# Optimization experiments

Measured on AMD Instinct MI355X. Metric: run time of the kernel, lower is better.

The kernel has to match this reference:

```python
import jax, jax.numpy as jnp
import numpy as np
from jax.scipy.linalg import solve_triangular


def setup_inputs() -> dict:
    B, L, H, Dv, Mh = 32, 1024, 12, 64, 64
    hdim = H * Dv
    key = jax.random.key(0)
    ks = jax.random.split(key, 6)
    x = jax.random.normal(ks[0], (B, L, hdim), jnp.float32)
    W_qv = jax.random.normal(ks[1], (2 * H * Dv, hdim), jnp.float32) * 0.02
    log_sf = jnp.zeros((H, 1), jnp.float32)
    log_ls = jnp.zeros((H, Dv), jnp.float32)
    log_sigma2 = jnp.asarray(-2.0, jnp.float32)
    omega = jax.random.normal(ks[2], (H, Dv, Mh), jnp.float32)
    omega_half, _ = jnp.linalg.qr(omega)  # per-head orthonormal columns, Dv >= Mh
    phase = 2.0 * np.pi * jax.random.uniform(ks[3], (H, Mh), jnp.float32)
    W_O_w = jax.random.normal(ks[4], (hdim, hdim), jnp.float32) * 0.02
    W_O_b = jnp.zeros((hdim,), jnp.float32)
    eps = jax.random.normal(ks[5], (B, H, 1, L, Dv), jnp.float32)  # sample_size=1
    return dict(x=x, W_qv=W_qv, log_sf=log_sf, log_ls=log_ls,
                log_sigma2=log_sigma2, omega_half=omega_half, phase=phase,
                W_O_w=W_O_w, W_O_b=W_O_b, eps=eps)


def reference(x, W_qv, log_sf, log_ls, log_sigma2, omega_half, phase, W_O_w, W_O_b, eps):
    B, L, hdim = x.shape
    H, Dv, Mh = omega_half.shape
    M = 2 * Mh
    jitter = 1e-06
    # fc_qv (no bias), split into q / v per head: [B,H,L,Dv]
    qv = (x @ W_qv.T).reshape(B, L, H, 2 * Dv).transpose(0, 2, 1, 3)
    q, v = qv[..., :Dv], qv[..., Dv:]
    # RFF feature map (ard kernel): phi [B,H,L,M]
    scale = jnp.sqrt(2.0) * jnp.exp(-log_ls)                  # [H,Dv]
    omega = omega_half * scale[:, :, None]                    # [H,Dv,Mh]
    proj = jnp.einsum('bhld,hdm->bhlm', q, omega) + phase[None, :, None, :]
    phi = jnp.concatenate([jnp.cos(proj), jnp.sin(proj)], axis=-1)
    amp = jnp.sqrt(jnp.exp(log_sf))[None, :, None, :]         # [1,H,1,1]
    phi = amp * phi * (1.0 / np.sqrt(M))
    sigma2 = jnp.exp(log_sigma2)
    # Gram + regularized Cholesky (upper R with A = R^T R; lower Lc = R^T)
    G = jnp.einsum('bhlm,bhln->bhmn', phi, phi)               # [B,H,M,M]
    I = jnp.eye(M, dtype=x.dtype)
    A = G + (sigma2 + jitter) * I
    Lc = jnp.linalg.cholesky(A)                               # lower
    R = jnp.swapaxes(Lc, -1, -2)                              # upper
    # whitened features: tQ = (R^-T phi^T)^T  (phi_q == phi_k)
    tQ = jnp.swapaxes(solve_triangular(Lc, jnp.swapaxes(phi, -1, -2), lower=True), -1, -2)
    S = jnp.einsum('bhlm,bhld->bhmd', tQ, v)                  # [B,H,M,Dv]
    mean_feat = jnp.einsum('bhlm,bhmd->bhld', tQ, S)          # [B,H,L,Dv]
    var_scalar = sigma2 * jnp.sum(tQ ** 2, axis=-1, keepdims=True)  # [B,H,L,1]
    std = jnp.sqrt(jnp.clip(var_scalar, 0.0))
    # sampling: [B,H,Smp,L,Dv] -> [B,Smp,L,H*Dv]
    samples = mean_feat[:, :, None] + std[:, :, None] * eps
    Smp = eps.shape[2]
    samples = samples.transpose(0, 2, 3, 1, 4).reshape(B, Smp, L, H * Dv)
    samples = samples @ W_O_w.T + W_O_b  # W_O (dropout = identity)
    # exact feature-space KL
    W_star = solve_triangular(R, S, lower=False)              # [B,H,M,Dv]
    mu_norm2 = jnp.sum(W_star ** 2, axis=(-2, -1))
    R_inv = solve_triangular(R, jnp.broadcast_to(I, A.shape), lower=False)
    tr_Ainv = jnp.sum(R_inv ** 2, axis=(-2, -1))
    logdetA = 2.0 * jnp.sum(jnp.log(jnp.diagonal(R, axis1=-2, axis2=-1)), axis=-1)
    k = M * Dv
    KL_bh = 0.5 * (Dv * sigma2 * tr_Ainv + mu_norm2 - k
                   - Dv * (M * jnp.log(sigma2) - logdetA))
    kl = KL_bh.sum(axis=1).mean()
    return samples, kl
```

## Files before the change

kernel.cpp:

```cpp
#include <hip/hip_runtime.h>
#include <hip/hip_bf16.h>
#include <math.h>

#define B_   32
#define L_   1024
#define H_   12
#define DV   64
#define MH   64
#define MM   128
#define HD   768
#define BH_  384

typedef unsigned int  uint32;
typedef unsigned short ushort16;
typedef __attribute__((ext_vector_type(4))) float f32x4;
typedef __attribute__((ext_vector_type(8))) short bf16x8;

__device__ __forceinline__ float bf2f(uint32 u) {
  return __uint_as_float(u << 16);
}
__device__ __forceinline__ ushort16 f2bf(float f) {
  uint32 x = __float_as_uint(f);
  x += 0x7FFFu + ((x >> 16) & 1u);
  return (ushort16)(x >> 16);
}
__device__ __forceinline__ uint32 pack2bf(float a, float b) {
  return (uint32)f2bf(a) | ((uint32)f2bf(b) << 16);
}

__global__ __launch_bounds__(256)
void k0_prep(const float* __restrict__ x, const float* __restrict__ Wqv,
             const float* __restrict__ omega_half, const float* __restrict__ log_ls,
             ushort16* __restrict__ xbf, ushort16* __restrict__ wqvbf,
             ushort16* __restrict__ omTbf, float* __restrict__ klbuf) {
  size_t i0 = (size_t)blockIdx.x * 256 + threadIdx.x;
  size_t stride = (size_t)gridDim.x * 256;
  for (size_t i = i0; i < (size_t)25165824 / 4; i += stride) {
    float4 v = ((const float4*)x)[i];
    uint2 w; w.x = pack2bf(v.x, v.y); w.y = pack2bf(v.z, v.w);
    ((uint2*)xbf)[i] = w;
  }
  for (size_t i = i0; i < (size_t)1179648 / 4; i += stride) {
    float4 v = ((const float4*)Wqv)[i];
    uint2 w; w.x = pack2bf(v.x, v.y); w.y = pack2bf(v.z, v.w);
    ((uint2*)wqvbf)[i] = w;
  }
  if (blockIdx.x < H_) {
    int h = blockIdx.x;
    for (int e = threadIdx.x; e < MH * DV; e += blockDim.x) {
      int m = e >> 6, d = e & 63;
      float scale = 1.41421356237f * expf(-log_ls[h * DV + d]);
      omTbf[h * MH * DV + m * DV + d] = f2bf(omega_half[h * DV * MH + d * MH + m] * scale);
    }
  }
  if (blockIdx.x == 0) {
    for (int e = threadIdx.x; e < BH_; e += blockDim.x) klbuf[e] = 0.f;
  }
}

__global__ __launch_bounds__(256)
void k1_qv_mfma(const ushort16* __restrict__ xbf, const ushort16* __restrict__ wqvbf,
                ushort16* __restrict__ qv) {
  __shared__ ushort16 As[128 * 40];
  __shared__ ushort16 Bs[128 * 40];
  int tid = threadIdx.x;
  int h  = blockIdx.x % 12;
  int tm = blockIdx.x / 12;
  int m0 = tm * 128;
  int n0 = h * 128;
  int wave = tid >> 6, lane = tid & 63;
  int wy = wave >> 1, wx = wave & 1;
  int mlane = lane & 15, q = lane >> 4;
  f32x4 acc[4][4];
#pragma unroll
  for (int i = 0; i < 4; i++)
#pragma unroll
    for (int j = 0; j < 4; j++) acc[i][j] = (f32x4){0.f, 0.f, 0.f, 0.f};

  int c0 = tid, c1 = tid + 256;
  int rowA0 = c0 >> 2, ka0 = (c0 & 3) * 8;
  int rowA1 = c1 >> 2, ka1 = (c1 & 3) * 8;

  for (int k0 = 0; k0 < HD; k0 += 32) {
    __syncthreads();
    uint4 a0 = *(const uint4*)&xbf[(size_t)(m0 + rowA0) * HD + k0 + ka0];
    uint4 a1 = *(const uint4*)&xbf[(size_t)(m0 + rowA1) * HD + k0 + ka1];
    uint4 b0 = *(const uint4*)&wqvbf[(size_t)(n0 + rowA0) * HD + k0 + ka0];
    uint4 b1 = *(const uint4*)&wqvbf[(size_t)(n0 + rowA1) * HD + k0 + ka1];
    *(uint4*)&As[rowA0 * 40 + ka0] = a0;
    *(uint4*)&As[rowA1 * 40 + ka1] = a1;
    *(uint4*)&Bs[rowA0 * 40 + ka0] = b0;
    *(uint4*)&Bs[rowA1 * 40 + ka1] = b1;
    __syncthreads();
    bf16x8 av[4], bv[4];
#pragma unroll
    for (int i = 0; i < 4; i++)
      av[i] = *(const bf16x8*)&As[(wy * 64 + i * 16 + mlane) * 40 + q * 8];
#pragma unroll
    for (int j = 0; j < 4; j++)
      bv[j] = *(const bf16x8*)&Bs[(wx * 64 + j * 16 + mlane) * 40 + q * 8];
#pragma unroll
    for (int i = 0; i < 4; i++)
#pragma unroll
      for (int j = 0; j < 4; j++)
        acc[i][j] = __builtin_amdgcn_mfma_f32_16x16x32_bf16(av[i], bv[j], acc[i][j], 0, 0, 0);
  }
#pragma unroll
  for (int i = 0; i < 4; i++) {
#pragma unroll
    for (int e = 0; e < 4; e++) {
      int gm = m0 + wy * 64 + i * 16 + q * 4 + e;
      int b = gm >> 10, l = gm & 1023;
      ushort16* dst = qv + ((((size_t)(b * 12 + h) << 10) | (unsigned)l) << 7);
#pragma unroll
      for (int j = 0; j < 4; j++) {
        int c = wx * 64 + j * 16 + mlane;
        dst[c] = f2bf(acc[i][j][e]);
      }
    }
  }
}

__global__ __launch_bounds__(256)
void k2_gram_mfma(const ushort16* __restrict__ qv, const ushort16* __restrict__ omTbf,
                  const float* __restrict__ phase, const float* __restrict__ log_sf,
                  char* __restrict__ Gbase, float* __restrict__ Cws) {
  __shared__ ushort16 PhT[128 * 136];
  __shared__ ushort16 vT[64 * 136];
  __shared__ float phaseS[MH];
  int bh = blockIdx.x;
  int h = bh % H_;
  int tid = threadIdx.x;
  int wave = tid >> 6, lane = tid & 63;
  int ml = lane & 15, qq = lane >> 4;
  if (tid < MH) phaseS[tid] = phase[h * MH + tid];
  float amp = sqrtf(expf(log_sf[h])) * 0.08838834764831845f;
  const ushort16* qp = qv + (size_t)bh * L_ * MM;
  const ushort16* Om = omTbf + h * MH * DV;
  f32x4 gacc[2][8];
  f32x4 cacc[2][4];
#pragma unroll
  for (int i = 0; i < 2; i++) {
#pragma unroll
    for (int j = 0; j < 8; j++) gacc[i][j] = (f32x4){0.f, 0.f, 0.f, 0.f};
#pragma unroll
    for (int j = 0; j < 4; j++) cacc[i][j] = (f32x4){0.f, 0.f, 0.f, 0.f};
  }
  __syncthreads();

  for (int l0 = 0; l0 < L_; l0 += 128) {
    f32x4 pacc[2][4];
#pragma unroll
    for (int i = 0; i < 2; i++)
#pragma unroll
      for (int j = 0; j < 4; j++) pacc[i][j] = (f32x4){0.f, 0.f, 0.f, 0.f};
#pragma unroll
    for (int k = 0; k < 2; k++) {
      bf16x8 af[2], bfm[4];
#pragma unroll
      for (int i = 0; i < 2; i++)
        af[i] = *(const bf16x8*)&qp[(size_t)(l0 + wave * 32 + i * 16 + ml) * MM + k * 32 + qq * 8];
#pragma unroll
      for (int j = 0; j < 4; j++)
        bfm[j] = *(const bf16x8*)&Om[(j * 16 + ml) * DV + k * 32 + qq * 8];
#pragma unroll
      for (int i = 0; i < 2; i++)
#pragma unroll
        for (int j = 0; j < 4; j++)
          pacc[i][j] = __builtin_amdgcn_mfma_f32_16x16x32_bf16(af[i], bfm[j], pacc[i][j], 0, 0, 0);
    }
    for (int u = tid; u < 1024; u += 256) {
      int row = u >> 3, g = u & 7;
      uint4 w = *(const uint4*)&qp[(size_t)(l0 + row) * MM + 64 + g * 8];
      vT[(g * 8 + 0) * 136 + row] = (ushort16)(w.x & 0xffffu);
      vT[(g * 8 + 1) * 136 + row] = (ushort16)(w.x >> 16);
      vT[(g * 8 + 2) * 136 + row] = (ushort16)(w.y & 0xffffu);
      vT[(g * 8 + 3) * 136 + row] = (ushort16)(w.y >> 16);
      vT[(g * 8 + 4) * 136 + row] = (ushort16)(w.z & 0xffffu);
      vT[(g * 8 + 5) * 136 + row] = (ushort16)(w.z >> 16);
      vT[(g * 8 + 6) * 136 + row] = (ushort16)(w.w & 0xffffu);
      vT[(g * 8 + 7) * 136 + row] = (ushort16)(w.w >> 16);
    }
#pragma unroll
    for (int i = 0; i < 2; i++)
#pragma unroll
      for (int j = 0; j < 4; j++)
#pragma unroll
        for (int e = 0; e < 4; e++) {
          int l = wave * 32 + i * 16 + qq * 4 + e;
          int m = j * 16 + ml;
          float s = pacc[i][j][e] + phaseS[m];
          float sv, cv;
          sincosf(s, &sv, &cv);
          PhT[m * 136 + l]        = f2bf(amp * cv);
          PhT[(MH + m) * 136 + l] = f2bf(amp * sv);
        }
    __syncthreads();
#pragma unroll
    for (int k = 0; k < 4; k++) {
      bf16x8 af[2];
#pragma unroll
      for (int i = 0; i < 2; i++)
        af[i] = *(const bf16x8*)&PhT[(wave * 32 + i * 16 + ml) * 136 + k * 32 + qq * 8];
#pragma unroll
      for (int j = 0; j < 8; j++) {
        bf16x8 bfr = *(const bf16x8*)&PhT[(j * 16 + ml) * 136 + k * 32 + qq * 8];
#pragma unroll
        for (int i = 0; i < 2; i++)
          gacc[i][j] = __builtin_amdgcn_mfma_f32_16x16x32_bf16(af[i], bfr, gacc[i][j], 0, 0, 0);
      }
#pragma unroll
      for (int j = 0; j < 4; j++) {
        bf16x8 bvr = *(const bf16x8*)&vT[(j * 16 + ml) * 136 + k * 32 + qq * 8];
#pragma unroll
        for (int i = 0; i < 2; i++)
          cacc[i][j] = __builtin_amdgcn_mfma_f32_16x16x32_bf16(af[i], bvr, cacc[i][j], 0, 0, 0);
      }
    }
    __syncthreads();
  }
  float* Gp = (float*)(Gbase + (size_t)bh * 65536);
#pragma unroll
  for (int i = 0; i < 2; i++)
#pragma unroll
    for (int e = 0; e < 4; e++) {
      int m = wave * 32 + i * 16 + qq * 4 + e;
#pragma unroll
      for (int j = 0; j < 8; j++) Gp[m * MM + j * 16 + ml] = gacc[i][j][e];
    }
  float* Cp = Cws + (size_t)bh * MM * DV;
#pragma unroll
  for (int i = 0; i < 2; i++)
#pragma unroll
    for (int e = 0; e < 4; e++) {
      int m = wave * 32 + i * 16 + qq * 4 + e;
#pragma unroll
      for (int j = 0; j < 4; j++) Cp[m * DV + j * 16 + ml] = cacc[i][j][e];
    }
}

#define LB_(i,k) LBs[((i) << 7) + (((k) + (i)) & 127)]

__global__ __launch_bounds__(256)
void k3_factor(char* __restrict__ Gbase,
               const float* __restrict__ log_sigma2, float* __restrict__ klbuf) {
  __shared__ float LBs[MM * MM];
  int bh = blockIdx.x;
  int tid = threadIdx.x;
  float ls = log_sigma2[0];
  float sigma2 = expf(ls);
  float cjit = sigma2 + 1e-6f;
  const float* Gp = (const float*)(Gbase + (size_t)bh * 65536);
  for (int e = tid; e < MM * MM; e += 256) {
    int m = e >> 7, n = e & 127;
    float g = Gp[e];
    if (m == n) g += cjit;
    LB_(m, n) = g;
  }
  float klp = 0.f;

  for (int P = 0; P < 8; P++) {
    int p0 = P * 16;
    __syncthreads();
    if (tid < 16) {
      int t = tid;
      float r[16];
#pragma unroll
      for (int k = 0; k < 16; k++) r[k] = LB_(p0 + t, p0 + k);
#pragma unroll
      for (int j = 0; j < 16; j++) {
        float djj = __shfl(r[j], j);
        float sd = sqrtf(djj);
        float rinv = 1.f / sd;
        if (t == j) r[j] = sd;
        else if (t > j) r[j] *= rinv;
#pragma unroll
        for (int k2 = 0; k2 < 16; k2++) {
          if (k2 > j) {
            float lkj = __shfl(r[j], k2);
            if (t >= k2) r[k2] = fmaf(-r[j], lkj, r[k2]);
          }
        }
      }
#pragma unroll
      for (int k = 0; k < 16; k++) if (k <= t) LB_(p0 + t, p0 + k) = r[k];
      klp += 64.f * logf(r[t]);
    }
    __syncthreads();
    int NR = 112 - p0;
    if (NR > 0 && tid < NR) {
      int gi = p0 + 16 + tid;
      float a[16];
#pragma unroll
      for (int k = 0; k < 16; k++) a[k] = LB_(gi, p0 + k);
#pragma unroll
      for (int j = 0; j < 16; j++) {
        float inv = 1.f / LB_(p0 + j, p0 + j);
        a[j] *= inv;
#pragma unroll
        for (int k = 0; k < 16; k++)
          if (k > j) a[k] = fmaf(-a[j], LB_(p0 + k, p0 + j), a[k]);
      }
#pragma unroll
      for (int k = 0; k < 16; k++) LB_(gi, p0 + k) = a[k];
    }
    __syncthreads();
    int S = NR;
    if (S > 0) {
      int base = p0 + 16;
      int t4 = S >> 2;
      int ntiles = t4 * t4;
      for (int tt = tid; tt < ntiles; tt += 256) {
        int ti = tt / t4, tj = tt % t4;
        if (ti < tj) continue;
        int gi = base + ti * 4, gj = base + tj * 4;
        float acc[4][4] = {};
#pragma unroll
        for (int j = 0; j < 16; j++) {
          float pa[4], pb[4];
#pragma unroll
          for (int a2 = 0; a2 < 4; a2++) pa[a2] = LB_(gi + a2, p0 + j);
#pragma unroll
          for (int b2 = 0; b2 < 4; b2++) pb[b2] = LB_(gj + b2, p0 + j);
#pragma unroll
          for (int a2 = 0; a2 < 4; a2++)
#pragma unroll
            for (int b2 = 0; b2 < 4; b2++)
              acc[a2][b2] = fmaf(pa[a2], pb[b2], acc[a2][b2]);
        }
#pragma unroll
        for (int a2 = 0; a2 < 4; a2++)
#pragma unroll
          for (int b2 = 0; b2 < 4; b2++)
            LB_(gi + a2, gj + b2) -= acc[a2][b2];
      }
    }
  }
  __syncthreads();

  {
    float xk[16];
    int cb = tid >> 4, cc = tid & 15;
    if (tid < 128) {
      int g = cb * 16;
#pragma unroll
      for (int rr = 0; rr < 16; rr++) {
        float s = (rr == cc) ? 1.f : 0.f;
#pragma unroll
        for (int k = 0; k < 16; k++)
          if (k < rr) s = fmaf(-LB_(g + rr, g + k), xk[k], s);
        xk[rr] = (rr >= cc) ? s / LB_(g + rr, g + rr) : 0.f;
      }
    }
    __syncthreads();
    if (tid < 128) {
      int g = cb * 16;
#pragma unroll
      for (int rr = 0; rr < 16; rr++) LB_(g + rr, g + cc) = xk[rr];
    }
    __syncthreads();
  }

  {
    int r16 = tid >> 4, c16 = tid & 15;
    for (int J = 6; J >= 0; J--) {
      int nb = 7 - J;
      float yv[7];
#pragma unroll
      for (int q = 0; q < 7; q++) {
        if (q < nb) {
          int K = J + 1 + q;
          float s = 0.f;
#pragma unroll
          for (int c2 = 0; c2 < 16; c2++)
            s = fmaf(LB_(K * 16 + r16, J * 16 + c2), LB_(J * 16 + c2, J * 16 + c16), s);
          yv[q] = s;
        }
      }
      __syncthreads();
#pragma unroll
      for (int q = 0; q < 7; q++)
        if (q < nb) LB_((J + 1 + q) * 16 + r16, J * 16 + c16) = yv[q];
      __syncthreads();
      float xv[7];
#pragma unroll
      for (int q = 0; q < 7; q++) {
        if (q < nb) {
          int I = J + 1 + q;
          float s = 0.f;
          for (int K = J + 1; K <= I; K++) {
#pragma unroll
            for (int k = 0; k < 16; k++)
              s = fmaf(LB_(I * 16 + r16, K * 16 + k), LB_(K * 16 + k, J * 16 + c16), s);
          }
          xv[q] = -s;
        }
      }
      __syncthreads();
#pragma unroll
      for (int q = 0; q < 7; q++)
        if (q < nb) LB_((J + 1 + q) * 16 + r16, J * 16 + c16) = xv[q];
      __syncthreads();
    }
  }

  ushort16* Xb = (ushort16*)(Gbase + (size_t)bh * 65536);
  for (int e = tid; e < MM * MM; e += 256) {
    int r = e >> 7, c = e & 127;
    float xv2 = (c <= r) ? LB_(r, c) : 0.f;
    Xb[e] = f2bf(xv2);
    klp += 32.f * sigma2 * xv2 * xv2;
  }
  if (tid == 0) klp += -4096.f - 4096.f * ls;
  atomicAdd(&klbuf[bh], klp);
}

__global__ __launch_bounds__(256)
void k3b_dw(const char* __restrict__ Gbase, const float* __restrict__ Cws,
            float* __restrict__ klbuf) {
  __shared__ ushort16 XTl[128 * 136];
  __shared__ ushort16 CTD[64 * 136];
  int bh = blockIdx.x;
  int tid = threadIdx.x;
  int wave = tid >> 6, lane = tid & 63;
  int ml = lane & 15, qq = lane >> 4;
  const ushort16* Xb = (const ushort16*)(Gbase + (size_t)bh * 65536);
  ushort16* DTb = (ushort16*)(Gbase + (size_t)bh * 65536 + 32768);
  const float* Cp = Cws + (size_t)bh * MM * DV;

  for (int e = tid; e < 1024; e += 256) {
    int m = e >> 3, g = e & 7;
    float4 w0 = *(const float4*)&Cp[m * 64 + g * 8];
    float4 w1 = *(const float4*)&Cp[m * 64 + g * 8 + 4];
    CTD[(g * 8 + 0) * 136 + m] = f2bf(w0.x);
    CTD[(g * 8 + 1) * 136 + m] = f2bf(w0.y);
    CTD[(g * 8 + 2) * 136 + m] = f2bf(w0.z);
    CTD[(g * 8 + 3) * 136 + m] = f2bf(w0.w);
    CTD[(g * 8 + 4) * 136 + m] = f2bf(w1.x);
    CTD[(g * 8 + 5) * 136 + m] = f2bf(w1.y);
    CTD[(g * 8 + 6) * 136 + m] = f2bf(w1.z);
    CTD[(g * 8 + 7) * 136 + m] = f2bf(w1.w);
  }
  for (int e = tid; e < 2048; e += 256) {
    int n = e >> 4, g = e & 15;
    uint4 w = *(const uint4*)&Xb[n * MM + g * 8];
    XTl[(g * 8 + 0) * 136 + n] = (ushort16)(w.x & 0xffffu);
    XTl[(g * 8 + 1) * 136 + n] = (ushort16)(w.x >> 16);
    XTl[(g * 8 + 2) * 136 + n] = (ushort16)(w.y & 0xffffu);
    XTl[(g * 8 + 3) * 136 + n] = (ushort16)(w.y >> 16);
    XTl[(g * 8 + 4) * 136 + n] = (ushort16)(w.z & 0xffffu);
    XTl[(g * 8 + 5) * 136 + n] = (ushort16)(w.z >> 16);
    XTl[(g * 8 + 6) * 136 + n] = (ushort16)(w.w & 0xffffu);
    XTl[(g * 8 + 7) * 136 + n] = (ushort16)(w.w >> 16);
  }
  __syncthreads();

  f32x4 dacc[2][4];
#pragma unroll
  for (int i = 0; i < 2; i++)
#pragma unroll
    for (int j = 0; j < 4; j++) dacc[i][j] = (f32x4){0.f, 0.f, 0.f, 0.f};
#pragma unroll
  for (int k = 0; k < 4; k++) {
    bf16x8 af[2];
#pragma unroll
    for (int i = 0; i < 2; i++)
      af[i] = *(const bf16x8*)&Xb[(wave * 32 + i * 16 + ml) * MM + k * 32 + qq * 8];
#pragma unroll
    for (int j = 0; j < 4; j++) {
      bf16x8 bfr = *(const bf16x8*)&CTD[(j * 16 + ml) * 136 + k * 32 + qq * 8];
#pragma unroll
      for (int i = 0; i < 2; i++)
        dacc[i][j] = __builtin_amdgcn_mfma_f32_16x16x32_bf16(af[i], bfr, dacc[i][j], 0, 0, 0);
    }
  }
  __syncthreads();

#pragma unroll
  for (int i = 0; i < 2; i++)
#pragma unroll
    for (int j = 0; j < 4; j++)
#pragma unroll
      for (int e = 0; e < 4; e++) {
        int n = wave * 32 + i * 16 + qq * 4 + e;
        int d = j * 16 + ml;
        CTD[d * 136 + n] = f2bf(dacc[i][j][e]);
      }
  __syncthreads();

  f32x4 wacc[8];
#pragma unroll
  for (int j = 0; j < 8; j++) wacc[j] = (f32x4){0.f, 0.f, 0.f, 0.f};
#pragma unroll
  for (int k = 0; k < 4; k++) {
    bf16x8 afD = *(const bf16x8*)&CTD[(wave * 16 + ml) * 136 + k * 32 + qq * 8];
#pragma unroll
    for (int j = 0; j < 8; j++) {
      bf16x8 bfX = *(const bf16x8*)&XTl[(j * 16 + ml) * 136 + k * 32 + qq * 8];
      wacc[j] = __builtin_amdgcn_mfma_f32_16x16x32_bf16(afD, bfX, wacc[j], 0, 0, 0);
    }
  }
  float klp = 0.f;
#pragma unroll
  for (int j = 0; j < 8; j++)
#pragma unroll
    for (int e = 0; e < 4; e++) klp += 0.5f * wacc[j][e] * wacc[j][e];
  klp += __shfl_xor(klp, 1);
  klp += __shfl_xor(klp, 2);
  klp += __shfl_xor(klp, 4);
  klp += __shfl_xor(klp, 8);
  klp += __shfl_xor(klp, 16);
  klp += __shfl_xor(klp, 32);
  if (lane == 0) atomicAdd(&klbuf[bh], klp);

  for (int u = tid; u < 1024; u += 256) {
    int d = u >> 4, g = u & 15;
    *(uint4*)&DTb[d * MM + g * 8] = *(const uint4*)&CTD[d * 136 + g * 8];
  }
}

__global__ __launch_bounds__(256)
void k4_sample_mfma(const ushort16* __restrict__ qv, const ushort16* __restrict__ omTbf,
                    const float* __restrict__ phase, const float* __restrict__ log_sf,
                    const float* __restrict__ log_sigma2, const char* __restrict__ Gbase,
                    const float* __restrict__ eps, ushort16* __restrict__ sfeat) {
  __shared__ ushort16 ABuf[128 * 136];
  __shared__ ushort16 obuf[128 * 72];
  __shared__ float stdS[128];
  __shared__ float phaseS[MH];
  int blk = blockIdx.x;
  int bh = blk >> 3, l0 = (blk & 7) << 7;
  int h = bh % H_, b = bh / H_;
  int tid = threadIdx.x;
  int wave = tid >> 6, lane = tid & 63;
  int ml = lane & 15, qq = lane >> 4;
  if (tid < MH) phaseS[tid] = phase[h * MH + tid];
  float amp = sqrtf(expf(log_sf[h])) * 0.08838834764831845f;
  float sigma2 = expf(log_sigma2[0]);
  const ushort16* qp = qv + ((size_t)bh * L_ + l0) * MM;
  const ushort16* Om = omTbf + h * MH * DV;
  const ushort16* Xb = (const ushort16*)(Gbase + (size_t)bh * 65536);
  const ushort16* DT = (const ushort16*)(Gbase + (size_t)bh * 65536 + 32768);

  f32x4 pacc[2][4];
#pragma unroll
  for (int i = 0; i < 2; i++)
#pragma unroll
    for (int j = 0; j < 4; j++) pacc[i][j] = (f32x4){0.f, 0.f, 0.f, 0.f};
#pragma unroll
  for (int k = 0; k < 2; k++) {
    bf16x8 af[2], bfm[4];
#pragma unroll
    for (int i = 0; i < 2; i++)
      af[i] = *(const bf16x8*)&qp[(size_t)(wave * 32 + i * 16 + ml) * MM + k * 32 + qq * 8];
#pragma unroll
    for (int j = 0; j < 4; j++)
      bfm[j] = *(const bf16x8*)&Om[(j * 16 + ml) * DV + k * 32 + qq * 8];
#pragma unroll
    for (int i = 0; i < 2; i++)
#pragma unroll
      for (int j = 0; j < 4; j++)
        pacc[i][j] = __builtin_amdgcn_mfma_f32_16x16x32_bf16(af[i], bfm[j], pacc[i][j], 0, 0, 0);
  }
  __syncthreads();
#pragma unroll
  for (int i = 0; i < 2; i++)
#pragma unroll
    for (int j = 0; j < 4; j++)
#pragma unroll
      for (int e = 0; e < 4; e++) {
        int l = wave * 32 + i * 16 + qq * 4 + e;
        int m = j * 16 + ml;
        float s = pacc[i][j][e] + phaseS[m];
        float sv, cv;
        sincosf(s, &sv, &cv);
        ABuf[l * 136 + m]      = f2bf(amp * cv);
        ABuf[l * 136 + 64 + m] = f2bf(amp * sv);
      }
  f32x4 zacc[2][8];
#pragma unroll
  for (int i = 0; i < 2; i++)
#pragma unroll
    for (int j = 0; j < 8; j++) zacc[i][j] = (f32x4){0.f, 0.f, 0.f, 0.f};
#pragma unroll
  for (int k = 0; k < 4; k++) {
    bf16x8 af[2];
#pragma unroll
    for (int i = 0; i < 2; i++)
      af[i] = *(const bf16x8*)&ABuf[(wave * 32 + i * 16 + ml) * 136 + k * 32 + qq * 8];
#pragma unroll
    for (int j = 0; j < 8; j++) {
      bf16x8 bfr = *(const bf16x8*)&Xb[(j * 16 + ml) * MM + k * 32 + qq * 8];
#pragma unroll
      for (int i = 0; i < 2; i++)
        zacc[i][j] = __builtin_amdgcn_mfma_f32_16x16x32_bf16(af[i], bfr, zacc[i][j], 0, 0, 0);
    }
  }
#pragma unroll
  for (int i = 0; i < 2; i++)
#pragma unroll
    for (int e = 0; e < 4; e++) {
      float vs = 0.f;
#pragma unroll
      for (int j = 0; j < 8; j++) vs += zacc[i][j][e] * zacc[i][j][e];
      vs += __shfl_xor(vs, 1);
      vs += __shfl_xor(vs, 2);
      vs += __shfl_xor(vs, 4);
      vs += __shfl_xor(vs, 8);
      if (ml == 0) stdS[wave * 32 + i * 16 + qq * 4 + e] = sqrtf(fmaxf(sigma2 * vs, 0.f));
    }
#pragma unroll
  for (int i = 0; i < 2; i++)
#pragma unroll
    for (int j = 0; j < 8; j++)
#pragma unroll
      for (int e = 0; e < 4; e++) {
        int l = wave * 32 + i * 16 + qq * 4 + e;
        ABuf[l * 136 + j * 16 + ml] = f2bf(zacc[i][j][e]);
      }
  f32x4 macc[2][4];
#pragma unroll
  for (int i = 0; i < 2; i++)
#pragma unroll
    for (int j = 0; j < 4; j++) macc[i][j] = (f32x4){0.f, 0.f, 0.f, 0.f};
#pragma unroll
  for (int k = 0; k < 4; k++) {
    bf16x8 af[2];
#pragma unroll
    for (int i = 0; i < 2; i++)
      af[i] = *(const bf16x8*)&ABuf[(wave * 32 + i * 16 + ml) * 136 + k * 32 + qq * 8];
#pragma unroll
    for (int j = 0; j < 4; j++) {
      bf16x8 bfr = *(const bf16x8*)&DT[(j * 16 + ml) * MM + k * 32 + qq * 8];
#pragma unroll
      for (int i = 0; i < 2; i++)
        macc[i][j] = __builtin_amdgcn_mfma_f32_16x16x32_bf16(af[i], bfr, macc[i][j], 0, 0, 0);
    }
  }
  const float* ep = eps + ((size_t)bh * L_ + l0) * DV;
#pragma unroll
  for (int i = 0; i < 2; i++)
#pragma unroll
    for (int j = 0; j < 4; j++)
#pragma unroll
      for (int e = 0; e < 4; e++) {
        int l = wave * 32 + i * 16 + qq * 4 + e;
        int d = j * 16 + ml;
        float smp = macc[i][j][e] + stdS[l] * ep[l * DV + d];
        obuf[l * 72 + d] = f2bf(smp);
      }
  __syncthreads();
  ushort16* sp = sfeat + ((size_t)b * L_ + l0) * HD + h * DV;
  for (int u = tid; u < 512; u += 256) {
    int row = u >> 2, part = u & 3;
    uint4 val = *(const uint4*)&obuf[row * 72 + part * 8];
    *(uint4*)&sp[(size_t)row * HD + part * 8] = val;
  }
}

__global__ __launch_bounds__(256)
void k5_out_mfma(const ushort16* __restrict__ sfeat, const float* __restrict__ Wo,
                 const float* __restrict__ bias, float* __restrict__ outp) {
  __shared__ ushort16 As[128 * 40];
  __shared__ ushort16 Bs[128 * 40];
  int tid = threadIdx.x;
  int tn = blockIdx.x % 6;
  int tm = blockIdx.x / 6;
  int m0 = tm * 128, n0 = tn * 128;
  int wave = tid >> 6, lane = tid & 63;
  int wy = wave >> 1, wx = wave & 1;
  int mlane = lane & 15, q = lane >> 4;
  f32x4 acc[4][4];
#pragma unroll
  for (int i = 0; i < 4; i++)
#pragma unroll
    for (int j = 0; j < 4; j++) acc[i][j] = (f32x4){0.f, 0.f, 0.f, 0.f};

  int c0 = tid, c1 = tid + 256;
  int rowA0 = c0 >> 2, ka0 = (c0 & 3) * 8;
  int rowA1 = c1 >> 2, ka1 = (c1 & 3) * 8;

  for (int k0 = 0; k0 < HD; k0 += 32) {
    __syncthreads();
    uint4 a0 = *(const uint4*)&sfeat[(size_t)(m0 + rowA0) * HD + k0 + ka0];
    uint4 a1 = *(const uint4*)&sfeat[(size_t)(m0 + rowA1) * HD + k0 + ka1];
    float4 w00 = *(const float4*)&Wo[(size_t)(n0 + rowA0) * HD + k0 + ka0];
    float4 w01 = *(const float4*)&Wo[(size_t)(n0 + rowA0) * HD + k0 + ka0 + 4];
    float4 w10 = *(const float4*)&Wo[(size_t)(n0 + rowA1) * HD + k0 + ka1];
    float4 w11 = *(const float4*)&Wo[(size_t)(n0 + rowA1) * HD + k0 + ka1 + 4];
    uint4 b0, b1;
    b0.x = pack2bf(w00.x, w00.y); b0.y = pack2bf(w00.z, w00.w);
    b0.z = pack2bf(w01.x, w01.y); b0.w = pack2bf(w01.z, w01.w);
    b1.x = pack2bf(w10.x, w10.y); b1.y = pack2bf(w10.z, w10.w);
    b1.z = pack2bf(w11.x, w11.y); b1.w = pack2bf(w11.z, w11.w);
    *(uint4*)&As[rowA0 * 40 + ka0] = a0;
    *(uint4*)&As[rowA1 * 40 + ka1] = a1;
    *(uint4*)&Bs[rowA0 * 40 + ka0] = b0;
    *(uint4*)&Bs[rowA1 * 40 + ka1] = b1;
    __syncthreads();
    bf16x8 av[4], bv[4];
#pragma unroll
    for (int i = 0; i < 4; i++)
      av[i] = *(const bf16x8*)&As[(wy * 64 + i * 16 + mlane) * 40 + q * 8];
#pragma unroll
    for (int j = 0; j < 4; j++)
      bv[j] = *(const bf16x8*)&Bs[(wx * 64 + j * 16 + mlane) * 40 + q * 8];
#pragma unroll
    for (int i = 0; i < 4; i++)
#pragma unroll
      for (int j = 0; j < 4; j++)
        acc[i][j] = __builtin_amdgcn_mfma_f32_16x16x32_bf16(av[i], bv[j], acc[i][j], 0, 0, 0);
  }
  float bsv[4];
#pragma unroll
  for (int j = 0; j < 4; j++) bsv[j] = bias[n0 + wx * 64 + j * 16 + mlane];
#pragma unroll
  for (int i = 0; i < 4; i++) {
#pragma unroll
    for (int e = 0; e < 4; e++) {
      int gm = m0 + wy * 64 + i * 16 + q * 4 + e;
#pragma unroll
      for (int j = 0; j < 4; j++) {
        int gn = n0 + wx * 64 + j * 16 + mlane;
        outp[(size_t)gm * HD + gn] = acc[i][j][e] + bsv[j];
      }
    }
  }
}

__global__ void k6_kl(const float* __restrict__ klbuf, float* __restrict__ outp) {
  __shared__ float red[2];
  int tid = threadIdx.x;
  float s = 0.f;
  for (int e = tid; e < BH_; e += 128) s += klbuf[e];
  for (int off = 32; off >= 1; off >>= 1) s += __shfl_xor(s, off);
  if ((tid & 63) == 0) red[tid >> 6] = s;
  __syncthreads();
  if (tid == 0) outp[(size_t)B_ * L_ * HD] = (red[0] + red[1]) * (1.f / 32.f);
}

extern "C" void kernel_launch(void* const* d_in, const int* in_sizes, int n_in,
                              void* d_out, int out_size, void* d_ws, size_t ws_size,
                              hipStream_t stream) {
  (void)in_sizes; (void)n_in; (void)out_size; (void)ws_size;
  const float* x       = (const float*)d_in[0];
  const float* Wqv     = (const float*)d_in[1];
  const float* log_sf  = (const float*)d_in[2];
  const float* log_ls  = (const float*)d_in[3];
  const float* log_s2  = (const float*)d_in[4];
  const float* omega_h = (const float*)d_in[5];
  const float* phase   = (const float*)d_in[6];
  const float* Wo      = (const float*)d_in[7];
  const float* Wob     = (const float*)d_in[8];
  const float* eps     = (const float*)d_in[9];
  float* outp = (float*)d_out;

  char* ws = (char*)d_ws;
  ushort16* qv    = (ushort16*)(ws);
  ushort16* xbf   = (ushort16*)(ws + 100663296);
  ushort16* sfeat = xbf;
  ushort16* omTbf = (ushort16*)(ws + 150994944);
  char*     Gbase = ws + 151191552;
  ushort16* wqvbf = (ushort16*)(ws + 151191552);
  float*    Cws   = (float*)(ws + 176357376);
  float*    klbuf = (float*)(ws + 188940288);

  hipLaunchKernelGGL(k0_prep,       dim3(1024), dim3(256), 0, stream, x, Wqv, omega_h, log_ls, xbf, wqvbf, omTbf, klbuf);
  hipLaunchKernelGGL(k1_qv_mfma,    dim3(3072), dim3(256), 0, stream, xbf, wqvbf, qv);
  hipLaunchKernelGGL(k2_gram_mfma,  dim3(BH_),  dim3(256), 0, stream, qv, omTbf, phase, log_sf, Gbase, Cws);
  hipLaunchKernelGGL(k3_factor,     dim3(BH_),  dim3(256), 0, stream, Gbase, log_s2, klbuf);
  hipLaunchKernelGGL(k3b_dw,        dim3(BH_),  dim3(256), 0, stream, Gbase, Cws, klbuf);
  hipLaunchKernelGGL(k4_sample_mfma,dim3(3072), dim3(256), 0, stream, qv, omTbf, phase, log_sf, log_s2, Gbase, eps, sfeat);
  hipLaunchKernelGGL(k5_out_mfma,   dim3(1536), dim3(256), 0, stream, sfeat, Wo, Wob, outp);
  hipLaunchKernelGGL(k6_kl,         dim3(1),    dim3(128), 0, stream, klbuf, outp);
}
```

Measured before the change: 893.4 us.

## Fuse x fp32-to-bf16 conversion into QV GEMM and widen K tile to 64

Drops the separate pass that converted x (about 100 MB fp32) to a bf16 copy in workspace. The QV GEMM now loads fp32 x directly and packs it to bf16 while staging into shared memory. Both GEMMs also move from a K step of 32 to 64, with padded LDS rows of 72, halving the number of barrier pairs. The cost is reading x at fp32 width inside the GEMM, where each x tile is re-read by the 12 head blocks (the reads should mostly hit cache), plus larger LDS use per block.

```diff
diff --git a/kernel.cpp b/kernel.cpp
--- a/kernel.cpp
+++ b/kernel.cpp
@@ -29,17 +29,12 @@
 }
 
 __global__ __launch_bounds__(256)
-void k0_prep(const float* __restrict__ x, const float* __restrict__ Wqv,
+void k0_prep(const float* __restrict__ Wqv,
              const float* __restrict__ omega_half, const float* __restrict__ log_ls,
-             ushort16* __restrict__ xbf, ushort16* __restrict__ wqvbf,
+             ushort16* __restrict__ wqvbf,
              ushort16* __restrict__ omTbf, float* __restrict__ klbuf) {
   size_t i0 = (size_t)blockIdx.x * 256 + threadIdx.x;
   size_t stride = (size_t)gridDim.x * 256;
-  for (size_t i = i0; i < (size_t)25165824 / 4; i += stride) {
-    float4 v = ((const float4*)x)[i];
-    uint2 w; w.x = pack2bf(v.x, v.y); w.y = pack2bf(v.z, v.w);
-    ((uint2*)xbf)[i] = w;
-  }
   for (size_t i = i0; i < (size_t)1179648 / 4; i += stride) {
     float4 v = ((const float4*)Wqv)[i];
     uint2 w; w.x = pack2bf(v.x, v.y); w.y = pack2bf(v.z, v.w);
@@ -59,10 +54,10 @@
 }
 
 __global__ __launch_bounds__(256)
-void k1_qv_mfma(const ushort16* __restrict__ xbf, const ushort16* __restrict__ wqvbf,
+void k1_qv_mfma(const float* __restrict__ x, const ushort16* __restrict__ wqvbf,
                 ushort16* __restrict__ qv) {
-  __shared__ ushort16 As[128 * 40];
-  __shared__ ushort16 Bs[128 * 40];
+  __shared__ ushort16 As[128 * 72];
+  __shared__ ushort16 Bs[128 * 72];
   int tid = threadIdx.x;
   int h  = blockIdx.x % 12;
   int tm = blockIdx.x / 12;
@@ -77,33 +72,51 @@
 #pragma unroll
     for (int j = 0; j < 4; j++) acc[i][j] = (f32x4){0.f, 0.f, 0.f, 0.f};
 
-  int c0 = tid, c1 = tid + 256;
-  int rowA0 = c0 >> 2, ka0 = (c0 & 3) * 8;
-  int rowA1 = c1 >> 2, ka1 = (c1 & 3) * 8;
-
-  for (int k0 = 0; k0 < HD; k0 += 32) {
-    __syncthreads();
-    uint4 a0 = *(const uint4*)&xbf[(size_t)(m0 + rowA0) * HD + k0 + ka0];
-    uint4 a1 = *(const uint4*)&xbf[(size_t)(m0 + rowA1) * HD + k0 + ka1];
-    uint4 b0 = *(const uint4*)&wqvbf[(size_t)(n0 + rowA0) * HD + k0 + ka0];
-    uint4 b1 = *(const uint4*)&wqvbf[(size_t)(n0 + rowA1) * HD + k0 + ka1];
-    *(uint4*)&As[rowA0 * 40 + ka0] = a0;
-    *(uint4*)&As[rowA1 * 40 + ka1] = a1;
-    *(uint4*)&Bs[rowA0 * 40 + ka0] = b0;
-    *(uint4*)&Bs[rowA1 * 40 + ka1] = b1;
-    __syncthreads();
-    bf16x8 av[4], bv[4];
-#pragma unroll
-    for (int i = 0; i < 4; i++)
-      av[i] = *(const bf16x8*)&As[(wy * 64 + i * 16 + mlane) * 40 + q * 8];
-#pragma unroll
-    for (int j = 0; j < 4; j++)
-      bv[j] = *(const bf16x8*)&Bs[(wx * 64 + j * 16 + mlane) * 40 + q * 8];
-#pragma unroll
-    for (int i = 0; i < 4; i++)
+  int rows[4], kgs[4];
+#pragma unroll
+  for (int t = 0; t < 4; t++) {
+    int c = tid + t * 256;
+    rows[t] = c >> 3;
+    kgs[t]  = (c & 7) * 8;
+  }
+
+  for (int k0 = 0; k0 < HD; k0 += 64) {
+    __syncthreads();
+    float4 af0[4], af1[4];
+    uint4 bv4[4];
+#pragma unroll
+    for (int t = 0; t < 4; t++) {
+      const float* ap = &x[(size_t)(m0 + rows[t]) * HD + k0 + kgs[t]];
+      af0[t] = *(const float4*)ap;
+      af1[t] = *(const float4*)(ap + 4);
+      bv4[t] = *(const uint4*)&wqvbf[(size_t)(n0 + rows[t]) * HD + k0 + kgs[t]];
+    }
+#pragma unroll
+    for (int t = 0; t < 4; t++) {
+      uint4 a4;
+      a4.x = pack2bf(af0[t].x, af0[t].y);
+      a4.y = pack2bf(af0[t].z, af0[t].w);
+      a4.z = pack2bf(af1[t].x, af1[t].y);
+      a4.w = pack2bf(af1[t].z, af1[t].w);
+      *(uint4*)&As[rows[t] * 72 + kgs[t]] = a4;
+      *(uint4*)&Bs[rows[t] * 72 + kgs[t]] = bv4[t];
+    }
+    __syncthreads();
+#pragma unroll
+    for (int kq = 0; kq < 2; kq++) {
+      bf16x8 av[4], bv[4];
+#pragma unroll
+      for (int i = 0; i < 4; i++)
+        av[i] = *(const bf16x8*)&As[(wy * 64 + i * 16 + mlane) * 72 + kq * 32 + q * 8];
 #pragma unroll
       for (int j = 0; j < 4; j++)
-        acc[i][j] = __builtin_amdgcn_mfma_f32_16x16x32_bf16(av[i], bv[j], acc[i][j], 0, 0, 0);
+        bv[j] = *(const bf16x8*)&Bs[(wx * 64 + j * 16 + mlane) * 72 + kq * 32 + q * 8];
+#pragma unroll
+      for (int i = 0; i < 4; i++)
+#pragma unroll
+        for (int j = 0; j < 4; j++)
+          acc[i][j] = __builtin_amdgcn_mfma_f32_16x16x32_bf16(av[i], bv[j], acc[i][j], 0, 0, 0);
+    }
   }
 #pragma unroll
   for (int i = 0; i < 4; i++) {
@@ -661,8 +674,8 @@
 __global__ __launch_bounds__(256)
 void k5_out_mfma(const ushort16* __restrict__ sfeat, const float* __restrict__ Wo,
                  const float* __restrict__ bias, float* __restrict__ outp) {
-  __shared__ ushort16 As[128 * 40];
-  __shared__ ushort16 Bs[128 * 40];
+  __shared__ ushort16 As[128 * 72];
+  __shared__ ushort16 Bs[128 * 72];
   int tid = threadIdx.x;
   int tn = blockIdx.x % 6;
   int tm = blockIdx.x / 6;
@@ -676,40 +689,51 @@
 #pragma unroll
     for (int j = 0; j < 4; j++) acc[i][j] = (f32x4){0.f, 0.f, 0.f, 0.f};
 
-  int c0 = tid, c1 = tid + 256;
-  int rowA0 = c0 >> 2, ka0 = (c0 & 3) * 8;
-  int rowA1 = c1 >> 2, ka1 = (c1 & 3) * 8;
-
-  for (int k0 = 0; k0 < HD; k0 += 32) {
-    __syncthreads();
-    uint4 a0 = *(const uint4*)&sfeat[(size_t)(m0 + rowA0) * HD + k0 + ka0];
-    uint4 a1 = *(const uint4*)&sfeat[(size_t)(m0 + rowA1) * HD + k0 + ka1];
-    float4 w00 = *(const float4*)&Wo[(size_t)(n0 + rowA0) * HD + k0 + ka0];
-    float4 w01 = *(const float4*)&Wo[(size_t)(n0 + rowA0) * HD + k0 + ka0 + 4];
-    float4 w10 = *(const float4*)&Wo[(size_t)(n0 + rowA1) * HD + k0 + ka1];
-    float4 w11 = *(const float4*)&Wo[(size_t)(n0 + rowA1) * HD + k0 + ka1 + 4];
-    uint4 b0, b1;
-    b0.x = pack2bf(w00.x, w00.y); b0.y = pack2bf(w00.z, w00.w);
-    b0.z = pack2bf(w01.x, w01.y); b0.w = pack2bf(w01.z, w01.w);
-    b1.x = pack2bf(w10.x, w10.y); b1.y = pack2bf(w10.z, w10.w);
-    b1.z = pack2bf(w11.x, w11.y); b1.w = pack2bf(w11.z, w11.w);
-    *(uint4*)&As[rowA0 * 40 + ka0] = a0;
-    *(uint4*)&As[rowA1 * 40 + ka1] = a1;
-    *(uint4*)&Bs[rowA0 * 40 + ka0] = b0;
-    *(uint4*)&Bs[rowA1 * 40 + ka1] = b1;
-    __syncthreads();
-    bf16x8 av[4], bv[4];
-#pragma unroll
-    for (int i = 0; i < 4; i++)
-      av[i] = *(const bf16x8*)&As[(wy * 64 + i * 16 + mlane) * 40 + q * 8];
-#pragma unroll
-    for (int j = 0; j < 4; j++)
-      bv[j] = *(const bf16x8*)&Bs[(wx * 64 + j * 16 + mlane) * 40 + q * 8];
-#pragma unroll
-    for (int i = 0; i < 4; i++)
+  int rows[4], kgs[4];
+#pragma unroll
+  for (int t = 0; t < 4; t++) {
+    int c = tid + t * 256;
+    rows[t] = c >> 3;
+    kgs[t]  = (c & 7) * 8;
+  }
+
+  for (int k0 = 0; k0 < HD; k0 += 64) {
+    __syncthreads();
+    uint4 av4[4];
+    float4 bf0[4], bf1[4];
+#pragma unroll
+    for (int t = 0; t < 4; t++) {
+      av4[t] = *(const uint4*)&sfeat[(size_t)(m0 + rows[t]) * HD + k0 + kgs[t]];
+      const float* bp = &Wo[(size_t)(n0 + rows[t]) * HD + k0 + kgs[t]];
+      bf0[t] = *(const float4*)bp;
+      bf1[t] = *(const float4*)(bp + 4);
+    }
+#pragma unroll
+    for (int t = 0; t < 4; t++) {
+      uint4 b4;
+      b4.x = pack2bf(bf0[t].x, bf0[t].y);
+      b4.y = pack2bf(bf0[t].z, bf0[t].w);
+      b4.z = pack2bf(bf1[t].x, bf1[t].y);
+      b4.w = pack2bf(bf1[t].z, bf1[t].w);
+      *(uint4*)&As[rows[t] * 72 + kgs[t]] = av4[t];
+      *(uint4*)&Bs[rows[t] * 72 + kgs[t]] = b4;
+    }
+    __syncthreads();
+#pragma unroll
+    for (int kq = 0; kq < 2; kq++) {
+      bf16x8 av[4], bv[4];
+#pragma unroll
+      for (int i = 0; i < 4; i++)
+        av[i] = *(const bf16x8*)&As[(wy * 64 + i * 16 + mlane) * 72 + kq * 32 + q * 8];
 #pragma unroll
       for (int j = 0; j < 4; j++)
-        acc[i][j] = __builtin_amdgcn_mfma_f32_16x16x32_bf16(av[i], bv[j], acc[i][j], 0, 0, 0);
+        bv[j] = *(const bf16x8*)&Bs[(wx * 64 + j * 16 + mlane) * 72 + kq * 32 + q * 8];
+#pragma unroll
+      for (int i = 0; i < 4; i++)
+#pragma unroll
+        for (int j = 0; j < 4; j++)
+          acc[i][j] = __builtin_amdgcn_mfma_f32_16x16x32_bf16(av[i], bv[j], acc[i][j], 0, 0, 0);
+    }
   }
   float bsv[4];
 #pragma unroll
@@ -757,16 +781,15 @@
 
   char* ws = (char*)d_ws;
   ushort16* qv    = (ushort16*)(ws);
-  ushort16* xbf   = (ushort16*)(ws + 100663296);
-  ushort16* sfeat = xbf;
+  ushort16* sfeat = (ushort16*)(ws + 100663296);
   ushort16* omTbf = (ushort16*)(ws + 150994944);
   char*     Gbase = ws + 151191552;
   ushort16* wqvbf = (ushort16*)(ws + 151191552);
   float*    Cws   = (float*)(ws + 176357376);
   float*    klbuf = (float*)(ws + 188940288);
 
-  hipLaunchKernelGGL(k0_prep,       dim3(1024), dim3(256), 0, stream, x, Wqv, omega_h, log_ls, xbf, wqvbf, omTbf, klbuf);
-  hipLaunchKernelGGL(k1_qv_mfma,    dim3(3072), dim3(256), 0, stream, xbf, wqvbf, qv);
+  hipLaunchKernelGGL(k0_prep,       dim3(1024), dim3(256), 0, stream, Wqv, omega_h, log_ls, wqvbf, omTbf, klbuf);
+  hipLaunchKernelGGL(k1_qv_mfma,    dim3(3072), dim3(256), 0, stream, x, wqvbf, qv);
   hipLaunchKernelGGL(k2_gram_mfma,  dim3(BH_),  dim3(256), 0, stream, qv, omTbf, phase, log_sf, Gbase, Cws);
   hipLaunchKernelGGL(k3_factor,     dim3(BH_),  dim3(256), 0, stream, Gbase, log_s2, klbuf);
   hipLaunchKernelGGL(k3b_dw,        dim3(BH_),  dim3(256), 0, stream, Gbase, Cws, klbuf);
```

New measurement: 903.8 us. Within noise of the previous version (+1.2%).

## Fuse x bf16 conversion into QV GEMM loads and merge Gram with Cholesky

Applied to the files above, without the earlier changes.

Removes the standalone pass converting x to bf16; the QV GEMM now loads fp32 x and packs to bf16 while staging tiles into shared memory. The Gram kernel and the factorization kernel are merged so the Gram accumulators go straight into the shared-memory factor buffer, avoiding a global write and reread of G. This trades some extra global read bandwidth in the GEMM (fp32 instead of bf16 operands) and a larger shared-memory footprint in the fused kernel.

```diff
diff --git a/kernel.cpp b/kernel.cpp
--- a/kernel.cpp
+++ b/kernel.cpp
@@ -29,17 +29,12 @@
 }
 
 __global__ __launch_bounds__(256)
-void k0_prep(const float* __restrict__ x, const float* __restrict__ Wqv,
+void k0_prep(const float* __restrict__ Wqv,
              const float* __restrict__ omega_half, const float* __restrict__ log_ls,
-             ushort16* __restrict__ xbf, ushort16* __restrict__ wqvbf,
+             ushort16* __restrict__ wqvbf,
              ushort16* __restrict__ omTbf, float* __restrict__ klbuf) {
   size_t i0 = (size_t)blockIdx.x * 256 + threadIdx.x;
   size_t stride = (size_t)gridDim.x * 256;
-  for (size_t i = i0; i < (size_t)25165824 / 4; i += stride) {
-    float4 v = ((const float4*)x)[i];
-    uint2 w; w.x = pack2bf(v.x, v.y); w.y = pack2bf(v.z, v.w);
-    ((uint2*)xbf)[i] = w;
-  }
   for (size_t i = i0; i < (size_t)1179648 / 4; i += stride) {
     float4 v = ((const float4*)Wqv)[i];
     uint2 w; w.x = pack2bf(v.x, v.y); w.y = pack2bf(v.z, v.w);
@@ -59,7 +54,7 @@
 }
 
 __global__ __launch_bounds__(256)
-void k1_qv_mfma(const ushort16* __restrict__ xbf, const ushort16* __restrict__ wqvbf,
+void k1_qv_mfma(const float* __restrict__ x, const ushort16* __restrict__ wqvbf,
                 ushort16* __restrict__ qv) {
   __shared__ ushort16 As[128 * 40];
   __shared__ ushort16 Bs[128 * 40];
@@ -83,10 +78,19 @@
 
   for (int k0 = 0; k0 < HD; k0 += 32) {
     __syncthreads();
-    uint4 a0 = *(const uint4*)&xbf[(size_t)(m0 + rowA0) * HD + k0 + ka0];
-    uint4 a1 = *(const uint4*)&xbf[(size_t)(m0 + rowA1) * HD + k0 + ka1];
+    const float* ap0 = &x[(size_t)(m0 + rowA0) * HD + k0 + ka0];
+    const float* ap1 = &x[(size_t)(m0 + rowA1) * HD + k0 + ka1];
+    float4 a00 = *(const float4*)ap0;
+    float4 a01 = *(const float4*)(ap0 + 4);
+    float4 a10 = *(const float4*)ap1;
+    float4 a11 = *(const float4*)(ap1 + 4);
     uint4 b0 = *(const uint4*)&wqvbf[(size_t)(n0 + rowA0) * HD + k0 + ka0];
     uint4 b1 = *(const uint4*)&wqvbf[(size_t)(n0 + rowA1) * HD + k0 + ka1];
+    uint4 a0, a1;
+    a0.x = pack2bf(a00.x, a00.y); a0.y = pack2bf(a00.z, a00.w);
+    a0.z = pack2bf(a01.x, a01.y); a0.w = pack2bf(a01.z, a01.w);
+    a1.x = pack2bf(a10.x, a10.y); a1.y = pack2bf(a10.z, a10.w);
+    a1.z = pack2bf(a11.x, a11.y); a1.w = pack2bf(a11.z, a11.w);
     *(uint4*)&As[rowA0 * 40 + ka0] = a0;
     *(uint4*)&As[rowA1 * 40 + ka1] = a1;
     *(uint4*)&Bs[rowA0 * 40 + ka0] = b0;
@@ -121,13 +125,19 @@
   }
 }
 
+#define LB_(i,k) LBs[((i) << 7) + (((k) + (i)) & 127)]
+
 __global__ __launch_bounds__(256)
-void k2_gram_mfma(const ushort16* __restrict__ qv, const ushort16* __restrict__ omTbf,
-                  const float* __restrict__ phase, const float* __restrict__ log_sf,
-                  char* __restrict__ Gbase, float* __restrict__ Cws) {
-  __shared__ ushort16 PhT[128 * 136];
-  __shared__ ushort16 vT[64 * 136];
+void k23_gram_factor(const ushort16* __restrict__ qv, const ushort16* __restrict__ omTbf,
+                     const float* __restrict__ phase, const float* __restrict__ log_sf,
+                     const float* __restrict__ log_sigma2,
+                     char* __restrict__ Gbase, float* __restrict__ Cws,
+                     float* __restrict__ klbuf) {
+  __shared__ char smem[65536];
   __shared__ float phaseS[MH];
+  ushort16* PhT = (ushort16*)smem;
+  ushort16* vT  = (ushort16*)(smem + 34816);
+  float*    LBs = (float*)smem;
   int bh = blockIdx.x;
   int h = bh % H_;
   int tid = threadIdx.x;
@@ -135,6 +145,9 @@
   int ml = lane & 15, qq = lane >> 4;
   if (tid < MH) phaseS[tid] = phase[h * MH + tid];
   float amp = sqrtf(expf(log_sf[h])) * 0.08838834764831845f;
+  float ls = log_sigma2[0];
+  float sigma2 = expf(ls);
+  float cjit = sigma2 + 1e-6f;
   const ushort16* qp = qv + (size_t)bh * L_ * MM;
   const ushort16* Om = omTbf + h * MH * DV;
   f32x4 gacc[2][8];
@@ -219,44 +232,28 @@
     }
     __syncthreads();
   }
-  float* Gp = (float*)(Gbase + (size_t)bh * 65536);
+  float* Cp = Cws + (size_t)bh * MM * DV;
 #pragma unroll
   for (int i = 0; i < 2; i++)
 #pragma unroll
     for (int e = 0; e < 4; e++) {
       int m = wave * 32 + i * 16 + qq * 4 + e;
 #pragma unroll
-      for (int j = 0; j < 8; j++) Gp[m * MM + j * 16 + ml] = gacc[i][j][e];
-    }
-  float* Cp = Cws + (size_t)bh * MM * DV;
+      for (int j = 0; j < 4; j++) Cp[m * DV + j * 16 + ml] = cacc[i][j][e];
+    }
 #pragma unroll
   for (int i = 0; i < 2; i++)
 #pragma unroll
     for (int e = 0; e < 4; e++) {
       int m = wave * 32 + i * 16 + qq * 4 + e;
 #pragma unroll
-      for (int j = 0; j < 4; j++) Cp[m * DV + j * 16 + ml] = cacc[i][j][e];
-    }
-}
-
-#define LB_(i,k) LBs[((i) << 7) + (((k) + (i)) & 127)]
-
-__global__ __launch_bounds__(256)
-void k3_factor(char* __restrict__ Gbase,
-               const float* __restrict__ log_sigma2, float* __restrict__ klbuf) {
-  __shared__ float LBs[MM * MM];
-  int bh = blockIdx.x;
-  int tid = threadIdx.x;
-  float ls = log_sigma2[0];
-  float sigma2 = expf(ls);
-  float cjit = sigma2 + 1e-6f;
-  const float* Gp = (const float*)(Gbase + (size_t)bh * 65536);
-  for (int e = tid; e < MM * MM; e += 256) {
-    int m = e >> 7, n = e & 127;
-    float g = Gp[e];
-    if (m == n) g += cjit;
-    LB_(m, n) = g;
-  }
+      for (int j = 0; j < 8; j++) {
+        int n = j * 16 + ml;
+        float g = gacc[i][j][e];
+        if (m == n) g += cjit;
+        LB_(m, n) = g;
+      }
+    }
   float klp = 0.f;
 
   for (int P = 0; P < 8; P++) {
@@ -757,20 +754,18 @@
 
   char* ws = (char*)d_ws;
   ushort16* qv    = (ushort16*)(ws);
-  ushort16* xbf   = (ushort16*)(ws + 100663296);
-  ushort16* sfeat = xbf;
+  ushort16* sfeat = (ushort16*)(ws + 100663296);
   ushort16* omTbf = (ushort16*)(ws + 150994944);
   char*     Gbase = ws + 151191552;
   ushort16* wqvbf = (ushort16*)(ws + 151191552);
   float*    Cws   = (float*)(ws + 176357376);
   float*    klbuf = (float*)(ws + 188940288);
 
-  hipLaunchKernelGGL(k0_prep,       dim3(1024), dim3(256), 0, stream, x, Wqv, omega_h, log_ls, xbf, wqvbf, omTbf, klbuf);
-  hipLaunchKernelGGL(k1_qv_mfma,    dim3(3072), dim3(256), 0, stream, xbf, wqvbf, qv);
-  hipLaunchKernelGGL(k2_gram_mfma,  dim3(BH_),  dim3(256), 0, stream, qv, omTbf, phase, log_sf, Gbase, Cws);
-  hipLaunchKernelGGL(k3_factor,     dim3(BH_),  dim3(256), 0, stream, Gbase, log_s2, klbuf);
-  hipLaunchKernelGGL(k3b_dw,        dim3(BH_),  dim3(256), 0, stream, Gbase, Cws, klbuf);
-  hipLaunchKernelGGL(k4_sample_mfma,dim3(3072), dim3(256), 0, stream, qv, omTbf, phase, log_sf, log_s2, Gbase, eps, sfeat);
-  hipLaunchKernelGGL(k5_out_mfma,   dim3(1536), dim3(256), 0, stream, sfeat, Wo, Wob, outp);
-  hipLaunchKernelGGL(k6_kl,         dim3(1),    dim3(128), 0, stream, klbuf, outp);
-}
+  hipLaunchKernelGGL(k0_prep,        dim3(1024), dim3(256), 0, stream, Wqv, omega_h, log_ls, wqvbf, omTbf, klbuf);
+  hipLaunchKernelGGL(k1_qv_mfma,     dim3(3072), dim3(256), 0, stream, x, wqvbf, qv);
+  hipLaunchKernelGGL(k23_gram_factor,dim3(BH_),  dim3(256), 0, stream, qv, omTbf, phase, log_sf, log_s2, Gbase, Cws, klbuf);
+  hipLaunchKernelGGL(k3b_dw,         dim3(BH_),  dim3(256), 0, stream, Gbase, Cws, klbuf);
+  hipLaunchKernelGGL(k4_sample_mfma, dim3(3072), dim3(256), 0, stream, qv, omTbf, phase, log_sf, log_s2, Gbase, eps, sfeat);
+  hipLaunchKernelGGL(k5_out_mfma,    dim3(1536), dim3(256), 0, stream, sfeat, Wo, Wob, outp);
+  hipLaunchKernelGGL(k6_kl,          dim3(1),    dim3(128), 0, stream, klbuf, outp);
+}
```

Result: slower. 997.6 us (+11.7%).
